# Performance work log

Hardware: AMD Instinct MI355X
Metric: run time of the kernel (lower is better)

## Reference

```python
import jax, jax.numpy as jnp
import numpy as np

N = 8192
LATENT_DIM = 64


def setup_inputs() -> dict:
    key = jax.random.key(0)
    kx, ky = jax.random.split(key)
    x = jax.random.normal(kx, (N, LATENT_DIM), dtype=jnp.float32)
    y = jax.random.normal(ky, (N, LATENT_DIM), dtype=jnp.float32)
    return {"x": x, "y": y}


def _rbf_kernel(a, b):
    # Faithful to torch: exp(-mean((a_i - b_j)^2, axis=dim) / dim)
    #                  = exp(-||a_i - b_j||^2 / dim^2)
    # Computed via the expanded-sq-dist identity to avoid the [N, N, dim]
    # tiled intermediate the torch code materializes.
    dim = a.shape[1]
    sq_a = jnp.sum(a * a, axis=1)  # [Na]
    sq_b = jnp.sum(b * b, axis=1)  # [Nb]
    sq_dist = sq_a[:, None] + sq_b[None, :] - 2.0 * (a @ b.T)  # [Na, Nb]
    return jnp.exp(-sq_dist / (dim * dim))


def reference(x, y):
    # MMD with RBF kernel: mean k(x,x) + mean k(y,y) - 2 mean k(x,y)
    kxx = jnp.mean(_rbf_kernel(x, x))
    kyy = jnp.mean(_rbf_kernel(y, y))
    kxy = jnp.mean(_rbf_kernel(x, y))
    return kxx + kyy - 2.0 * kxy
```

## Files before the change

### kernel.cpp

```cpp
#include <hip/hip_runtime.h>
#include <cmath>

#define NPTS 8192
#define DIM 64
#define BT 128
#define KSTR 132

#define LEAF_F   0
#define LEAF_N   (3 * 8192 * 64)
#define ROWS_F   (LEAF_F + LEAF_N)
#define ROWS_N   (3 * 8192)
#define MEANS_F  (ROWS_F + ROWS_N)
#define CNT_F    (MEANS_F + 3)
#define NX_F     ((CNT_F + 1 + 3) & ~3)
#define NY_F     (NX_F + 8192)
#define SPLIT_F  (NY_F + 8192)
#define SPLIT_ELEMS (NPTS * DIM)


typedef short bf16x8 __attribute__((ext_vector_type(8)));
typedef float f32x4  __attribute__((ext_vector_type(4)));

__device__ __forceinline__ unsigned short f32_bf16_rne(float f) {
    unsigned u = __float_as_uint(f);
    return (unsigned short)((u + 0x7FFFu + ((u >> 16) & 1u)) >> 16);
}
__device__ __forceinline__ float bf16_f32(unsigned short h) {
    return __uint_as_float(((unsigned)h) << 16);
}

__global__ void prep_kernel(const float* __restrict__ x, const float* __restrict__ y,
                            unsigned short* __restrict__ Xh, unsigned short* __restrict__ Xl,
                            unsigned short* __restrict__ Yh, unsigned short* __restrict__ Yl,
                            float* __restrict__ nx, float* __restrict__ ny,
                            unsigned* __restrict__ cnt) {
    int r = blockIdx.x * 64 + threadIdx.x;
    if (r == 0) *cnt = 0u;
    int isY = r >= NPTS;
    int rr = isY ? r - NPTS : r;
    const float4* Rg = (const float4*)((isY ? y : x) + (size_t)rr * DIM);
    unsigned short* Hh = isY ? Yh : Xh;
    unsigned short* Hl = isY ? Yl : Xl;
    const int t16 = rr >> 4, mrow = rr & 15;
    float s = 0.f;
    #pragma unroll
    for (int k4 = 0; k4 < 16; ++k4) {
        float4 v = Rg[k4];
        ushort4 h, l;
        h.x = f32_bf16_rne(v.x); l.x = f32_bf16_rne(v.x - bf16_f32(h.x));
        h.y = f32_bf16_rne(v.y); l.y = f32_bf16_rne(v.y - bf16_f32(h.y));
        h.z = f32_bf16_rne(v.z); l.z = f32_bf16_rne(v.z - bf16_f32(h.z));
        h.w = f32_bf16_rne(v.w); l.w = f32_bf16_rne(v.w - bf16_f32(h.w));
        int off = t16 * 1024 + (k4 >> 3) * 512 + ((k4 >> 1) & 3) * 128 + mrow * 8 + (k4 & 1) * 4;
        *(ushort4*)(Hh + off) = h;
        *(ushort4*)(Hl + off) = l;
        s = fmaf(v.x, v.x, s); s = fmaf(v.y, v.y, s);
        s = fmaf(v.z, v.z, s); s = fmaf(v.w, v.w, s);
    }
    if (isY) ny[rr] = s; else nx[rr] = s;
}

__global__ __launch_bounds__(512, 4) void mmd_tile_kernel(
    const unsigned short* __restrict__ Xh, const unsigned short* __restrict__ Xl,
    const unsigned short* __restrict__ Yh, const unsigned short* __restrict__ Yl,
    const float* __restrict__ nx, const float* __restrict__ ny,
    float* __restrict__ leafs)
{
    const int gi = blockIdx.x;
    const int gj = blockIdx.y;
    int zz, bx, by;
    if (blockIdx.z == 1) {
        if (gi >= 64) return;
        zz = 2; bx = gi; by = gj;
    } else if (gi > gj) {
        zz = 0; by = gj; bx = gi - 1;
    } else {
        zz = 1; by = gi; bx = gj;
    }

    __shared__ float Ks[128 * KSTR];
    __shared__ float sqA[BT];
    __shared__ float sqB[BT];

    const int t = threadIdx.x;
    const size_t arow = (size_t)by * BT;
    const size_t brow = (size_t)bx * BT;
    const int cb = bx;

    const unsigned short* pAh = (zz == 1) ? Yh : Xh;
    const unsigned short* pAl = (zz == 1) ? Yl : Xl;
    const unsigned short* pBh = (zz == 0) ? Xh : Yh;
    const unsigned short* pBl = (zz == 0) ? Xl : Yl;

    if (t < 256) {
        const float* nA = (zz == 1) ? ny : nx;
        const float* nB = (zz == 0) ? nx : ny;
        if (t < BT) sqA[t] = nA[arow + t];
        else        sqB[t - BT] = nB[brow + t - BT];
    }
    __syncthreads();

    const int lane = t & 63;
    const int wv   = t >> 6;
    const int mrow = lane & 15;
    const int quad = lane >> 4;
    const int rblk = (wv & 3) << 5;
    const int cblk = (wv >> 2) << 6;

    const int aT = by * 8 + (wv & 3) * 2;
    const int bT = bx * 8 + (wv >> 2) * 4;
    const int lsub = quad * 128 + mrow * 8;

    bf16x8 fAh[2][2], fAl[2][2];
    #pragma unroll
    for (int rt = 0; rt < 2; ++rt)
        #pragma unroll
        for (int kc = 0; kc < 2; ++kc) {
            int off = (aT + rt) * 1024 + kc * 512 + lsub;
            fAh[rt][kc] = *(const bf16x8*)(pAh + off);
            fAl[rt][kc] = *(const bf16x8*)(pAl + off);
        }

    f32x4 acc[2][4];
    #pragma unroll
    for (int rt = 0; rt < 2; ++rt)
        #pragma unroll
        for (int ct = 0; ct < 4; ++ct)
            acc[rt][ct] = (f32x4){0.f, 0.f, 0.f, 0.f};

    #pragma unroll
    for (int ct = 0; ct < 4; ++ct) {
        int boff = (bT + ct) * 1024 + lsub;
        bf16x8 bh0 = *(const bf16x8*)(pBh + boff);
        bf16x8 bh1 = *(const bf16x8*)(pBh + boff + 512);
        bf16x8 bl0 = *(const bf16x8*)(pBl + boff);
        bf16x8 bl1 = *(const bf16x8*)(pBl + boff + 512);
        #pragma unroll
        for (int rt = 0; rt < 2; ++rt) {
            f32x4 c = acc[rt][ct];
            c = __builtin_amdgcn_mfma_f32_16x16x32_bf16(fAh[rt][0], bh0, c, 0, 0, 0);
            c = __builtin_amdgcn_mfma_f32_16x16x32_bf16(fAh[rt][0], bl0, c, 0, 0, 0);
            c = __builtin_amdgcn_mfma_f32_16x16x32_bf16(fAl[rt][0], bh0, c, 0, 0, 0);
            c = __builtin_amdgcn_mfma_f32_16x16x32_bf16(fAh[rt][1], bh1, c, 0, 0, 0);
            c = __builtin_amdgcn_mfma_f32_16x16x32_bf16(fAh[rt][1], bl1, c, 0, 0, 0);
            c = __builtin_amdgcn_mfma_f32_16x16x32_bf16(fAl[rt][1], bh1, c, 0, 0, 0);
            acc[rt][ct] = c;
        }
    }

    const float SCL = (float)(-1.4426950408889634 / 4096.0);
    #pragma unroll
    for (int rt = 0; rt < 2; ++rt)
        #pragma unroll
        for (int ct = 0; ct < 4; ++ct)
            #pragma unroll
            for (int i = 0; i < 4; ++i) {
                int row = rblk + rt * 16 + quad * 4 + i;
                int col = cblk + ct * 16 + mrow;
                float d  = acc[rt][ct][i];
                float s2 = sqA[row] + sqB[col];
                float sqd = s2 - 2.0f * d;
                Ks[row * KSTR + col] = exp2f(sqd * SCL);
            }
    __syncthreads();

    float leaf[2];
    #pragma unroll
    for (int j = 0; j < 2; ++j) {
        int ch  = t + 512 * j;
        int row = ch >> 3;
        int tt  = ch & 7;
        float s = Ks[row * KSTR + tt];
        #pragma unroll
        for (int q = 1; q < 16; ++q) s += Ks[row * KSTR + tt + 8 * q];
        float p;
        p = __shfl_xor(s, 1); s = s + p;
        p = __shfl_xor(s, 2); s = s + p;
        p = __shfl_xor(s, 4); s = s + p;
        leaf[j] = s;
    }
    if ((t & 7) == 0) {
        int rb = t >> 3;
        #pragma unroll
        for (int j = 0; j < 2; ++j) {
            int row = rb + 64 * j;
            leafs[((size_t)zz * 64 + cb) * 8192 + arow + row] = leaf[j];
        }
    }

    if (zz < 2 && bx > by) {
        float mleaf[2];
        #pragma unroll
        for (int j = 0; j < 2; ++j) {
            int ch  = t + 512 * j;
            int c   = ch >> 3;
            int tt  = ch & 7;
            float s = Ks[tt * KSTR + c];
            #pragma unroll
            for (int q = 1; q < 16; ++q) s += Ks[(tt + 8 * q) * KSTR + c];
            float p;
            p = __shfl_xor(s, 1); s = s + p;
            p = __shfl_xor(s, 2); s = s + p;
            p = __shfl_xor(s, 4); s = s + p;
            mleaf[j] = s;
        }
        if ((t & 7) == 0) {
            int rb = t >> 3;
            #pragma unroll
            for (int j = 0; j < 2; ++j) {
                int row = rb + 64 * j;
                leafs[((size_t)zz * 64 + by) * 8192 + brow + row] = mleaf[j];
            }
        }
    }
}

__global__ void reduce_kernel(const float* __restrict__ leafs, float* __restrict__ rowsums,
                              unsigned* __restrict__ cnt, float* __restrict__ out) {
    __shared__ float L[256];
    __shared__ float M[3];
    __shared__ int lastFlag;
    const int t = threadIdx.x;
    const int tid = blockIdx.x * 256 + t;
    const int z = tid >> 13;
    const int r = tid & 8191;

    const float* base = leafs + ((size_t)z * 64) * 8192 + r;
    float v[64];
    #pragma unroll
    for (int cbi = 0; cbi < 64; ++cbi) v[cbi] = base[(size_t)cbi * 8192];
    #pragma unroll
    for (int n = 32; n >= 1; n >>= 1)
        #pragma unroll
        for (int i = 0; i < 64; ++i)
            if (i < n) v[i] = v[2*i] + v[2*i+1];
    rowsums[tid] = v[0];

    __threadfence();
    if (t == 0) {
        unsigned old = atomicAdd(cnt, 1u);
        lastFlag = (old == 95u) ? 1 : 0;
    }
    __syncthreads();
    if (!lastFlag) return;
    __threadfence();

    for (int zz = 0; zz < 3; ++zz) {
        const float4* src = (const float4*)(rowsums + zz * 8192);
        float w[32];
        #pragma unroll
        for (int i = 0; i < 8; ++i) {
            float4 q = src[t * 8 + i];
            w[4*i+0] = q.x; w[4*i+1] = q.y; w[4*i+2] = q.z; w[4*i+3] = q.w;
        }
        #pragma unroll
        for (int n = 16; n >= 1; n >>= 1)
            #pragma unroll
            for (int i = 0; i < 32; ++i)
                if (i < n) w[i] = w[2*i] + w[2*i+1];
        L[t] = w[0];
        __syncthreads();
        for (int n = 128; n >= 1; n >>= 1) {
            float u = 0.f;
            if (t < n) u = L[2*t] + L[2*t+1];
            __syncthreads();
            if (t < n) L[t] = u;
            __syncthreads();
        }
        if (t == 0) M[zz] = L[0] * (1.0f / 67108864.0f);
        __syncthreads();
    }
    if (t == 0) {
        float t1 = M[0] + M[1];
        out[0] = t1 - 2.0f * M[2];
    }
}

extern "C" void kernel_launch(void* const* d_in, const int* in_sizes, int n_in,
                              void* d_out, int out_size, void* d_ws, size_t ws_size,
                              hipStream_t stream) {
    const float* x = (const float*)d_in[0];
    const float* y = (const float*)d_in[1];
    float* wsf     = (float*)d_ws;
    float* leafs   = wsf + LEAF_F;
    float* rowsums = wsf + ROWS_F;
    unsigned* cnt  = (unsigned*)(wsf + CNT_F);
    float* nx      = wsf + NX_F;
    float* ny      = wsf + NY_F;
    unsigned short* Xh = (unsigned short*)(wsf + SPLIT_F);
    unsigned short* Xl = Xh + SPLIT_ELEMS;
    unsigned short* Yh = Xl + SPLIT_ELEMS;
    unsigned short* Yl = Yh + SPLIT_ELEMS;

    prep_kernel<<<256, 64, 0, stream>>>(x, y, Xh, Xl, Yh, Yl, nx, ny, cnt);
    dim3 grid(65, 64, 2);
    mmd_tile_kernel<<<grid, 512, 0, stream>>>(Xh, Xl, Yh, Yl, nx, ny, leafs);
    reduce_kernel<<<96, 256, 0, stream>>>(leafs, rowsums, cnt, (float*)d_out);
}
```

Before: 160.7 us.

## Halve LDS tile buffer with two-phase exp/reduce to raise tile-kernel occupancy

The 128x128 exp tile is now staged through LDS in two 64-row halves, cutting shared memory per block from about 67KB to about 34KB. Launch bounds move from 4 to 6 blocks per SIMD so more workgroups can be resident. The MFMA loop is reordered to iterate over k-chunks outermost and loads A fragments per chunk, which lowers the number of live registers. The mirror column sums are split into two partial passes, which adds extra __syncthreads barriers. prep_kernel is relaunched as 64 blocks of 256 threads instead of 256 blocks of 64.

```diff
diff --git a/kernel.cpp b/kernel.cpp
--- a/kernel.cpp
+++ b/kernel.cpp
@@ -34,7 +34,7 @@
                             unsigned short* __restrict__ Yh, unsigned short* __restrict__ Yl,
                             float* __restrict__ nx, float* __restrict__ ny,
                             unsigned* __restrict__ cnt) {
-    int r = blockIdx.x * 64 + threadIdx.x;
+    int r = blockIdx.x * 256 + threadIdx.x;
     if (r == 0) *cnt = 0u;
     int isY = r >= NPTS;
     int rr = isY ? r - NPTS : r;
@@ -60,7 +60,7 @@
     if (isY) ny[rr] = s; else nx[rr] = s;
 }
 
-__global__ __launch_bounds__(512, 4) void mmd_tile_kernel(
+__global__ __launch_bounds__(512, 6) void mmd_tile_kernel(
     const unsigned short* __restrict__ Xh, const unsigned short* __restrict__ Xl,
     const unsigned short* __restrict__ Yh, const unsigned short* __restrict__ Yl,
     const float* __restrict__ nx, const float* __restrict__ ny,
@@ -78,7 +78,7 @@
         zz = 1; by = gi; bx = gj;
     }
 
-    __shared__ float Ks[128 * KSTR];
+    __shared__ float Ks[64 * KSTR];
     __shared__ float sqA[BT];
     __shared__ float sqB[BT];
 
@@ -111,16 +111,6 @@
     const int bT = bx * 8 + (wv >> 2) * 4;
     const int lsub = quad * 128 + mrow * 8;
 
-    bf16x8 fAh[2][2], fAl[2][2];
-    #pragma unroll
-    for (int rt = 0; rt < 2; ++rt)
-        #pragma unroll
-        for (int kc = 0; kc < 2; ++kc) {
-            int off = (aT + rt) * 1024 + kc * 512 + lsub;
-            fAh[rt][kc] = *(const bf16x8*)(pAh + off);
-            fAl[rt][kc] = *(const bf16x8*)(pAl + off);
-        }
-
     f32x4 acc[2][4];
     #pragma unroll
     for (int rt = 0; rt < 2; ++rt)
@@ -129,47 +119,54 @@
             acc[rt][ct] = (f32x4){0.f, 0.f, 0.f, 0.f};
 
     #pragma unroll
-    for (int ct = 0; ct < 4; ++ct) {
-        int boff = (bT + ct) * 1024 + lsub;
-        bf16x8 bh0 = *(const bf16x8*)(pBh + boff);
-        bf16x8 bh1 = *(const bf16x8*)(pBh + boff + 512);
-        bf16x8 bl0 = *(const bf16x8*)(pBl + boff);
-        bf16x8 bl1 = *(const bf16x8*)(pBl + boff + 512);
+    for (int kc = 0; kc < 2; ++kc) {
+        bf16x8 a_h[2], a_l[2];
         #pragma unroll
         for (int rt = 0; rt < 2; ++rt) {
-            f32x4 c = acc[rt][ct];
-            c = __builtin_amdgcn_mfma_f32_16x16x32_bf16(fAh[rt][0], bh0, c, 0, 0, 0);
-            c = __builtin_amdgcn_mfma_f32_16x16x32_bf16(fAh[rt][0], bl0, c, 0, 0, 0);
-            c = __builtin_amdgcn_mfma_f32_16x16x32_bf16(fAl[rt][0], bh0, c, 0, 0, 0);
-            c = __builtin_amdgcn_mfma_f32_16x16x32_bf16(fAh[rt][1], bh1, c, 0, 0, 0);
-            c = __builtin_amdgcn_mfma_f32_16x16x32_bf16(fAh[rt][1], bl1, c, 0, 0, 0);
-            c = __builtin_amdgcn_mfma_f32_16x16x32_bf16(fAl[rt][1], bh1, c, 0, 0, 0);
-            acc[rt][ct] = c;
+            int off = (aT + rt) * 1024 + kc * 512 + lsub;
+            a_h[rt] = *(const bf16x8*)(pAh + off);
+            a_l[rt] = *(const bf16x8*)(pAl + off);
+        }
+        #pragma unroll
+        for (int ct = 0; ct < 4; ++ct) {
+            int boff = (bT + ct) * 1024 + kc * 512 + lsub;
+            bf16x8 b_h = *(const bf16x8*)(pBh + boff);
+            bf16x8 b_l = *(const bf16x8*)(pBl + boff);
+            #pragma unroll
+            for (int rt = 0; rt < 2; ++rt) {
+                f32x4 c = acc[rt][ct];
+                c = __builtin_amdgcn_mfma_f32_16x16x32_bf16(a_h[rt], b_h, c, 0, 0, 0);
+                c = __builtin_amdgcn_mfma_f32_16x16x32_bf16(a_h[rt], b_l, c, 0, 0, 0);
+                c = __builtin_amdgcn_mfma_f32_16x16x32_bf16(a_l[rt], b_h, c, 0, 0, 0);
+                acc[rt][ct] = c;
+            }
         }
     }
 
     const float SCL = (float)(-1.4426950408889634 / 4096.0);
-    #pragma unroll
-    for (int rt = 0; rt < 2; ++rt)
-        #pragma unroll
-        for (int ct = 0; ct < 4; ++ct)
-            #pragma unroll
-            for (int i = 0; i < 4; ++i) {
-                int row = rblk + rt * 16 + quad * 4 + i;
-                int col = cblk + ct * 16 + mrow;
-                float d  = acc[rt][ct][i];
-                float s2 = sqA[row] + sqB[col];
-                float sqd = s2 - 2.0f * d;
-                Ks[row * KSTR + col] = exp2f(sqd * SCL);
-            }
-    __syncthreads();
-
-    float leaf[2];
-    #pragma unroll
-    for (int j = 0; j < 2; ++j) {
-        int ch  = t + 512 * j;
-        int row = ch >> 3;
-        int tt  = ch & 7;
+    const bool domirror = (zz < 2) && (bx > by);
+    float mpart[2] = {0.f, 0.f};
+
+    if (rblk < 64) {
+        #pragma unroll
+        for (int rt = 0; rt < 2; ++rt)
+            #pragma unroll
+            for (int ct = 0; ct < 4; ++ct)
+                #pragma unroll
+                for (int i = 0; i < 4; ++i) {
+                    int row = rblk + rt * 16 + quad * 4 + i;
+                    int col = cblk + ct * 16 + mrow;
+                    float d  = acc[rt][ct][i];
+                    float s2 = sqA[row] + sqB[col];
+                    float sqd = s2 - 2.0f * d;
+                    Ks[row * KSTR + col] = exp2f(sqd * SCL);
+                }
+    }
+    __syncthreads();
+
+    {
+        int row = t >> 3;
+        int tt  = t & 7;
         float s = Ks[row * KSTR + tt];
         #pragma unroll
         for (int q = 1; q < 16; ++q) s += Ks[row * KSTR + tt + 8 * q];
@@ -177,39 +174,74 @@
         p = __shfl_xor(s, 1); s = s + p;
         p = __shfl_xor(s, 2); s = s + p;
         p = __shfl_xor(s, 4); s = s + p;
-        leaf[j] = s;
-    }
-    if ((t & 7) == 0) {
-        int rb = t >> 3;
+        if ((t & 7) == 0)
+            leafs[((size_t)zz * 64 + cb) * 8192 + arow + row] = s;
+    }
+    if (domirror) {
         #pragma unroll
         for (int j = 0; j < 2; ++j) {
-            int row = rb + 64 * j;
-            leafs[((size_t)zz * 64 + cb) * 8192 + arow + row] = leaf[j];
-        }
-    }
-
-    if (zz < 2 && bx > by) {
-        float mleaf[2];
+            int mc = t + 512 * j;
+            int c  = mc >> 3;
+            int tt = mc & 7;
+            float s = Ks[tt * KSTR + c];
+            #pragma unroll
+            for (int q = 1; q < 8; ++q) s += Ks[(tt + 8 * q) * KSTR + c];
+            mpart[j] = s;
+        }
+    }
+    __syncthreads();
+
+    if (rblk >= 64) {
+        #pragma unroll
+        for (int rt = 0; rt < 2; ++rt)
+            #pragma unroll
+            for (int ct = 0; ct < 4; ++ct)
+                #pragma unroll
+                for (int i = 0; i < 4; ++i) {
+                    int row = rblk + rt * 16 + quad * 4 + i;
+                    int col = cblk + ct * 16 + mrow;
+                    float d  = acc[rt][ct][i];
+                    float s2 = sqA[row] + sqB[col];
+                    float sqd = s2 - 2.0f * d;
+                    Ks[(row - 64) * KSTR + col] = exp2f(sqd * SCL);
+                }
+    }
+    __syncthreads();
+
+    {
+        int row = 64 + (t >> 3);
+        int tt  = t & 7;
+        float s = Ks[(row - 64) * KSTR + tt];
+        #pragma unroll
+        for (int q = 1; q < 16; ++q) s += Ks[(row - 64) * KSTR + tt + 8 * q];
+        float p;
+        p = __shfl_xor(s, 1); s = s + p;
+        p = __shfl_xor(s, 2); s = s + p;
+        p = __shfl_xor(s, 4); s = s + p;
+        if ((t & 7) == 0)
+            leafs[((size_t)zz * 64 + cb) * 8192 + arow + row] = s;
+    }
+    if (domirror) {
         #pragma unroll
         for (int j = 0; j < 2; ++j) {
-            int ch  = t + 512 * j;
-            int c   = ch >> 3;
-            int tt  = ch & 7;
-            float s = Ks[tt * KSTR + c];
-            #pragma unroll
-            for (int q = 1; q < 16; ++q) s += Ks[(tt + 8 * q) * KSTR + c];
+            int mc = t + 512 * j;
+            int c  = mc >> 3;
+            int tt = mc & 7;
+            float s = mpart[j];
+            #pragma unroll
+            for (int q = 8; q < 16; ++q) s += Ks[(tt + 8 * q - 64) * KSTR + c];
             float p;
             p = __shfl_xor(s, 1); s = s + p;
             p = __shfl_xor(s, 2); s = s + p;
             p = __shfl_xor(s, 4); s = s + p;
-            mleaf[j] = s;
+            mpart[j] = s;
         }
         if ((t & 7) == 0) {
             int rb = t >> 3;
             #pragma unroll
             for (int j = 0; j < 2; ++j) {
                 int row = rb + 64 * j;
-                leafs[((size_t)zz * 64 + by) * 8192 + brow + row] = mleaf[j];
+                leafs[((size_t)zz * 64 + by) * 8192 + brow + row] = mpart[j];
             }
         }
     }
@@ -292,7 +324,7 @@
     unsigned short* Yh = Xl + SPLIT_ELEMS;
     unsigned short* Yl = Yh + SPLIT_ELEMS;
 
-    prep_kernel<<<256, 64, 0, stream>>>(x, y, Xh, Xl, Yh, Yl, nx, ny, cnt);
+    prep_kernel<<<64, 256, 0, stream>>>(x, y, Xh, Xl, Yh, Yl, nx, ny, cnt);
     dim3 grid(65, 64, 2);
     mmd_tile_kernel<<<grid, 512, 0, stream>>>(Xh, Xl, Yh, Yl, nx, ny, leafs);
     reduce_kernel<<<96, 256, 0, stream>>>(leafs, rowsums, cnt, (float*)d_out);
```

Measured after the change: 172.3 us. +7.2%, slower.
